# Performance work log

Hardware: AMD Instinct MI355X
Metric: run time of the kernel (lower is better)

Reference implementation:

```python
import jax, jax.numpy as jnp
import numpy as np

N, F_IN, HID, EMB, K = 4096, 1433, 256, 16, 10
ALPHA = 0.2   # LeakyReLU negative slope
V = 1.0       # Student-t degrees of freedom
NEG_INF = -9e15


def _xavier(key, shape):
    std = (2.0 / (shape[0] + shape[1])) ** 0.5
    return std * jax.random.normal(key, shape, dtype=jnp.float32)


def setup_inputs() -> dict:
    key = jax.random.key(0)
    ks = jax.random.split(key, 10)
    x = jax.random.normal(ks[0], (N, F_IN), dtype=jnp.float32)
    adj = (jax.random.uniform(ks[1], (N, N)) < 0.01).astype(jnp.float32)
    adj = jnp.maximum(adj, jnp.eye(N, dtype=jnp.float32))
    M = jax.random.uniform(ks[2], (N, N), dtype=jnp.float32)  # proximity matrix
    return {
        "x": x,
        "adj": adj,
        "M": M,
        "W1": _xavier(ks[3], (F_IN, HID)),
        "a_self1": _xavier(ks[4], (HID, 1)),
        "a_neigh1": _xavier(ks[5], (HID, 1)),
        "W2": _xavier(ks[6], (HID, EMB)),
        "a_self2": _xavier(ks[7], (EMB, 1)),
        "a_neigh2": _xavier(ks[8], (EMB, 1)),
        "cluster_layer": _xavier(ks[9], (K, EMB)),
    }


def _gat_layer(h_in, adj, M, W, a_self, a_neigh):
    h = h_in @ W                                   # [N, D]
    # dense attention logits: self score broadcast over rows + neighbor score over cols
    logits = (h @ a_self) + (h @ a_neigh).T        # [N, N]
    logits = jax.nn.leaky_relu(logits * M, negative_slope=ALPHA)
    logits = jnp.where(adj > 0, logits, NEG_INF)
    attention = jax.nn.softmax(logits, axis=1)     # row-stochastic
    return jax.nn.elu(attention @ h)               # concat=True -> ELU


def reference(x, adj, M, W1, a_self1, a_neigh1, W2, a_self2, a_neigh2, cluster_layer):
    h = _gat_layer(x, adj, M, W1, a_self1, a_neigh1)
    h = _gat_layer(h, adj, M, W2, a_self2, a_neigh2)
    # F.normalize(h, p=2, dim=1) with eps clamp
    z = h / jnp.maximum(jnp.linalg.norm(h, axis=1, keepdims=True), 1e-12)
    A_pred = jax.nn.sigmoid(z @ z.T)               # [N, N] dot-product decoder
    # Student-t soft assignment (get_Q)
    dist2 = jnp.sum((z[:, None, :] - cluster_layer[None, :, :]) ** 2, axis=2)  # [N, K]
    q = 1.0 / (1.0 + dist2 / V)
    q = q ** ((V + 1.0) / 2.0)
    q = q / jnp.sum(q, axis=1, keepdims=True)
    return A_pred, z, q
```

## Files before the change

### kernel.cpp

```cpp
#include <hip/hip_runtime.h>
#include <hip/hip_bf16.h>

#define NN 4096
#define FIN 1433
#define HID 256
#define EMB 16
#define KCL 10
#define CAP 256
#define ALPHA_LR 0.2f
#define KP 1472
#define NT (KP / 64)

typedef __attribute__((ext_vector_type(8))) short bf16x8;
typedef __attribute__((ext_vector_type(8))) short s16x8;
typedef __attribute__((ext_vector_type(4))) float f32x4;

__device__ __align__(16) short g_xb[(size_t)NN * KP];
__device__ __align__(16) short g_w1t[(size_t)HID * KP];
__device__ __align__(16) float g_h1[(size_t)NN * HID];
__device__ __align__(16) float g_s1[NN];
__device__ __align__(16) float g_n1[NN];
__device__ __align__(16) int   g_cnt[NN];
__device__ __align__(16) int   g_cols[(size_t)NN * CAP];
__device__ __align__(16) float g_mv[(size_t)NN * CAP];
__device__ __align__(16) float g_h2[(size_t)NN * EMB];
__device__ __align__(16) float g_s2[NN];
__device__ __align__(16) float g_n2[NN];
__device__ __align__(16) float g_z[(size_t)NN * EMB];

__device__ __forceinline__ short f2bf(float f) {
    union { float f; unsigned u; } v; v.f = f;
    unsigned r = v.u + 0x7fffu + ((v.u >> 16) & 1u);
    return (short)(r >> 16);
}
__device__ __forceinline__ float eluf(float v) { return v > 0.f ? v : __expf(v) - 1.f; }

__launch_bounds__(256)
__global__ void k_cast(const float* __restrict__ x, const float* __restrict__ W1) {
    int b = blockIdx.x, tid = threadIdx.x;
    if (b < NN) {
        const float* src = x + (size_t)b * FIN;
        short* dst = g_xb + (size_t)b * KP;
        for (int j = tid; j < KP; j += 256)
            dst[j] = (j < FIN) ? f2bf(src[j]) : (short)0;
    } else {
        int n = b - NN;
        short* dst = g_w1t + (size_t)n * KP;
        for (int k = tid; k < KP; k += 256)
            dst[k] = (k < FIN) ? f2bf(W1[(size_t)k * HID + n]) : (short)0;
    }
}

__launch_bounds__(256)
__global__ void k_gemm1b() {
    __shared__ short As[2][32][72];
    __shared__ short Bs[2][64][72];
    int bid = blockIdx.x;
    int rt = bid >> 2, nt = bid & 3;
    int row0 = rt * 32, n0 = nt * 64;
    int tid = threadIdx.x, lane = tid & 63, w = tid >> 6;
    int wm = w >> 1, wn = w & 1;
    int arow = tid >> 3, acol = (tid & 7) * 8;
    int brow = tid >> 2, bcol = (tid & 3) * 16;
    const short* xptr = g_xb  + (size_t)(row0 + arow) * KP + acol;
    const short* wptr = g_w1t + (size_t)(n0 + brow) * KP + bcol;
    f32x4 acc0 = {0.f,0.f,0.f,0.f}, acc1 = {0.f,0.f,0.f,0.f};

    s16x8 a_r  = *(const s16x8*)xptr;
    s16x8 b_r0 = *(const s16x8*)wptr;
    s16x8 b_r1 = *(const s16x8*)(wptr + 8);
    *(s16x8*)&As[0][arow][acol]     = a_r;
    *(s16x8*)&Bs[0][brow][bcol]     = b_r0;
    *(s16x8*)&Bs[0][brow][bcol + 8] = b_r1;
    __syncthreads();

    int fr = lane & 15, fk = (lane >> 4) * 8;
    for (int t = 0; t < NT; ++t) {
        int cur = t & 1;
        if (t + 1 < NT) {
            a_r  = *(const s16x8*)(xptr + (t + 1) * 64);
            b_r0 = *(const s16x8*)(wptr + (t + 1) * 64);
            b_r1 = *(const s16x8*)(wptr + (t + 1) * 64 + 8);
        }
        #pragma unroll
        for (int kk = 0; kk < 2; ++kk) {
            bf16x8 af  = *(const bf16x8*)&As[cur][wm * 16 + fr][fk + kk * 32];
            bf16x8 bf0 = *(const bf16x8*)&Bs[cur][wn * 32 + fr][fk + kk * 32];
            bf16x8 bf1 = *(const bf16x8*)&Bs[cur][wn * 32 + 16 + fr][fk + kk * 32];
            acc0 = __builtin_amdgcn_mfma_f32_16x16x32_bf16(af, bf0, acc0, 0, 0, 0);
            acc1 = __builtin_amdgcn_mfma_f32_16x16x32_bf16(af, bf1, acc1, 0, 0, 0);
        }
        if (t + 1 < NT) {
            *(s16x8*)&As[cur ^ 1][arow][acol]     = a_r;
            *(s16x8*)&Bs[cur ^ 1][brow][bcol]     = b_r0;
            *(s16x8*)&Bs[cur ^ 1][brow][bcol + 8] = b_r1;
            __syncthreads();
        }
    }
    int rowb = (lane >> 4) * 4;
    #pragma unroll
    for (int t = 0; t < 4; ++t) {
        int grow = row0 + wm * 16 + rowb + t;
        g_h1[(size_t)grow * HID + n0 + wn * 32 + fr]      = acc0[t];
        g_h1[(size_t)grow * HID + n0 + wn * 32 + 16 + fr] = acc1[t];
    }
}

__launch_bounds__(256)
__global__ void k_sn1(const float* __restrict__ a_s, const float* __restrict__ a_n) {
    int row = blockIdx.x * 4 + (threadIdx.x >> 6);
    int lane = threadIdx.x & 63;
    const float* r = g_h1 + (size_t)row * HID;
    float ss = 0.f, sn = 0.f;
    #pragma unroll
    for (int q = 0; q < 4; ++q) {
        float hv = r[lane + 64 * q];
        ss += hv * a_s[lane + 64 * q];
        sn += hv * a_n[lane + 64 * q];
    }
    #pragma unroll
    for (int o = 32; o; o >>= 1) { ss += __shfl_xor(ss, o); sn += __shfl_xor(sn, o); }
    if (lane == 0) { g_s1[row] = ss; g_n1[row] = sn; }
}

__launch_bounds__(256)
__global__ void k_attn1s(const float* __restrict__ adj, const float* __restrict__ M,
                         const float* __restrict__ W2,
                         const float* __restrict__ as2, const float* __restrict__ an2) {
    __shared__ int lc[4][CAP];
    __shared__ int cnts[4];
    int w = threadIdx.x >> 6, lane = threadIdx.x & 63;
    int row = blockIdx.x * 4 + w;
    if (lane == 0) cnts[w] = 0;
    __syncthreads();

    const float* Arow = adj + (size_t)row * NN;
    #pragma unroll
    for (int it = 0; it < 16; it += 8) {
        f32x4 A[8];
        #pragma unroll
        for (int u = 0; u < 8; ++u)
            A[u] = *(const f32x4*)&Arow[(it + u) * 256 + lane * 4];
        #pragma unroll
        for (int u = 0; u < 8; ++u) {
            int j0 = (it + u) * 256 + lane * 4;
            #pragma unroll
            for (int q = 0; q < 4; ++q) {
                if (A[u][q] > 0.f) {
                    int pos = atomicAdd(&cnts[w], 1);
                    if (pos < CAP) lc[w][pos] = j0 + q;
                }
            }
        }
    }
    __syncthreads();
    int nnzC = cnts[w]; if (nnzC > CAP) nnzC = CAP;
    if (lane == 0) g_cnt[row] = nnzC;

    const float* Mrow = M + (size_t)row * NN;
    float s_i = g_s1[row];
    int c0 = 0, c1 = 0;
    float lg0 = -INFINITY, lg1 = -INFINITY;
    #pragma unroll
    for (int t = 0; t < 4; ++t) {
        int k = lane + 64 * t;
        if (k < nnzC) {
            int c = lc[w][k];
            float mv = Mrow[c];
            g_cols[(size_t)row * CAP + k] = c;
            g_mv[(size_t)row * CAP + k]   = mv;
            if (t < 2) {
                float tt = (s_i + g_n1[c]) * mv;
                float lg = tt > 0.f ? tt : ALPHA_LR * tt;
                if (t == 0) { c0 = c; lg0 = lg; } else { c1 = c; lg1 = lg; }
            }
        }
    }
    int nnz = nnzC > 128 ? 128 : nnzC;

    float mx = fmaxf(lg0, lg1);
    #pragma unroll
    for (int o = 32; o; o >>= 1) mx = fmaxf(mx, __shfl_xor(mx, o));
    float p0 = (lane < nnz)      ? __expf(lg0 - mx) : 0.f;
    float p1 = (lane + 64 < nnz) ? __expf(lg1 - mx) : 0.f;
    float sm = p0 + p1;
    #pragma unroll
    for (int o = 32; o; o >>= 1) sm += __shfl_xor(sm, o);
    float inv = 1.f / sm;

    f32x4 acc = {0.f, 0.f, 0.f, 0.f};
    int kmax = nnz < 64 ? nnz : 64;
    #pragma unroll 4
    for (int k = 0; k < kmax; ++k) {
        float p = __shfl(p0, k);
        int   c = __shfl(c0, k);
        acc += p * *(const f32x4*)&g_h1[(size_t)c * HID + lane * 4];
    }
    if (nnz > 64) {
        int k2 = nnz - 64;
        #pragma unroll 4
        for (int k = 0; k < k2; ++k) {
            float p = __shfl(p1, k);
            int   c = __shfl(c1, k);
            acc += p * *(const f32x4*)&g_h1[(size_t)c * HID + lane * 4];
        }
    }
    f32x4 o1;
    #pragma unroll
    for (int j = 0; j < 4; ++j) o1[j] = eluf(acc[j] * inv);

    float part[16];
    #pragma unroll
    for (int e = 0; e < 16; ++e) part[e] = 0.f;
    #pragma unroll
    for (int j = 0; j < 4; ++j) {
        const f32x4* wr = (const f32x4*)&W2[(size_t)(lane * 4 + j) * EMB];
        f32x4 w0 = wr[0], w1 = wr[1], w2 = wr[2], w3 = wr[3];
        float ov = o1[j];
        #pragma unroll
        for (int e = 0; e < 4; ++e) {
            part[e]      += ov * w0[e];
            part[4 + e]  += ov * w1[e];
            part[8 + e]  += ov * w2[e];
            part[12 + e] += ov * w3[e];
        }
    }
    #pragma unroll
    for (int o = 32; o; o >>= 1)
        #pragma unroll
        for (int e = 0; e < 16; ++e) part[e] += __shfl_xor(part[e], o);
    if (lane == 0) {
        float ps = 0.f, pn = 0.f;
        float* h2p = g_h2 + (size_t)row * EMB;
        #pragma unroll
        for (int e = 0; e < 16; ++e) {
            h2p[e] = part[e];
            ps += part[e] * as2[e];
            pn += part[e] * an2[e];
        }
        g_s2[row] = ps; g_n2[row] = pn;
    }
}

__launch_bounds__(256)
__global__ void k_attn2s(const float* __restrict__ cl,
                         float* __restrict__ zo, float* __restrict__ qo) {
    int row = blockIdx.x * 4 + (threadIdx.x >> 6);
    int lane = threadIdx.x & 63;
    int kq = lane >> 4, c = lane & 15;
    int nnz = g_cnt[row];
    float s_i = g_s2[row];
    const int* cp = g_cols + (size_t)row * CAP;
    const float* mp = g_mv + (size_t)row * CAP;
    float mx = -INFINITY;
    for (int k = kq; k < nnz; k += 4) {
        float t = (s_i + g_n2[cp[k]]) * mp[k];
        mx = fmaxf(mx, t > 0.f ? t : ALPHA_LR * t);
    }
    mx = fmaxf(mx, __shfl_xor(mx, 16));
    mx = fmaxf(mx, __shfl_xor(mx, 32));
    float l = 0.f, acc = 0.f;
    for (int k = kq; k < nnz; k += 4) {
        int colk = cp[k];
        float t = (s_i + g_n2[colk]) * mp[k];
        float p = __expf((t > 0.f ? t : ALPHA_LR * t) - mx);
        l += p;
        acc += p * g_h2[(size_t)colk * EMB + c];
    }
    l += __shfl_xor(l, 16);  l += __shfl_xor(l, 32);
    acc += __shfl_xor(acc, 16); acc += __shfl_xor(acc, 32);
    float h = eluf(acc / l);
    float ss = h * h;
    ss += __shfl_xor(ss, 1); ss += __shfl_xor(ss, 2);
    ss += __shfl_xor(ss, 4); ss += __shfl_xor(ss, 8);
    float z = h * (1.f / fmaxf(sqrtf(ss), 1e-12f));
    if (kq == 0) { g_z[(size_t)row * EMB + c] = z; zo[(size_t)row * EMB + c] = z; }
    float qv[KCL]; float qs = 0.f;
    #pragma unroll
    for (int k2 = 0; k2 < KCL; ++k2) {
        float d = z - cl[k2 * EMB + c];
        float d2 = d * d;
        d2 += __shfl_xor(d2, 1); d2 += __shfl_xor(d2, 2);
        d2 += __shfl_xor(d2, 4); d2 += __shfl_xor(d2, 8);
        float t = 1.f / (1.f + d2);
        qv[k2] = t; qs += t;
    }
    if (kq == 0 && c < KCL) {
        float myq = 0.f;
        #pragma unroll
        for (int k2 = 0; k2 < KCL; ++k2) if (c == k2) myq = qv[k2];
        qo[(size_t)row * KCL + c] = myq / qs;
    }
}

__launch_bounds__(256)
__global__ void k_apred(float* __restrict__ out) {
    __shared__ float za[128][17];
    __shared__ float zb[128][17];
    int bx = blockIdx.x & 31, by = blockIdx.x >> 5;
    int tid = threadIdx.x;
    {
        int idx = tid * 8;
        int row = idx >> 4;
        int e = idx & 15;
        const f32x4* sa = (const f32x4*)(g_z + (size_t)(by * 128 + row) * EMB + e);
        const f32x4* sb = (const f32x4*)(g_z + (size_t)(bx * 128 + row) * EMB + e);
        f32x4 a0 = sa[0], a1 = sa[1], b0 = sb[0], b1 = sb[1];
        #pragma unroll
        for (int t = 0; t < 4; ++t) {
            za[row][e + t] = a0[t]; za[row][e + 4 + t] = a1[t];
            zb[row][e + t] = b0[t]; zb[row][e + 4 + t] = b1[t];
        }
    }
    __syncthreads();
    int tr = tid >> 4, tc = tid & 15;
    float acc[8][8];
    #pragma unroll
    for (int r = 0; r < 8; ++r)
        #pragma unroll
        for (int c = 0; c < 8; ++c) acc[r][c] = 0.f;
    for (int e = 0; e < 16; ++e) {
        float ra[8], rb[8];
        #pragma unroll
        for (int r = 0; r < 8; ++r) ra[r] = za[tr * 8 + r][e];
        #pragma unroll
        for (int c = 0; c < 8; ++c) rb[c] = zb[tc * 8 + c][e];
        #pragma unroll
        for (int r = 0; r < 8; ++r)
            #pragma unroll
            for (int c = 0; c < 8; ++c) acc[r][c] += ra[r] * rb[c];
    }
    #pragma unroll
    for (int r = 0; r < 8; ++r) {
        f32x4 lo, hi;
        #pragma unroll
        for (int c = 0; c < 4; ++c) {
            lo[c] = 1.f / (1.f + __expf(-acc[r][c]));
            hi[c] = 1.f / (1.f + __expf(-acc[r][c + 4]));
        }
        float* dst = &out[(size_t)(by * 128 + tr * 8 + r) * NN + bx * 128 + tc * 8];
        *(f32x4*)dst = lo;
        *(f32x4*)(dst + 4) = hi;
    }
}

extern "C" void kernel_launch(void* const* d_in, const int* in_sizes, int n_in,
                              void* d_out, int out_size, void* d_ws, size_t ws_size,
                              hipStream_t stream) {
    (void)in_sizes; (void)n_in; (void)d_ws; (void)ws_size; (void)out_size;
    const float* x   = (const float*)d_in[0];
    const float* adj = (const float*)d_in[1];
    const float* M   = (const float*)d_in[2];
    const float* W1  = (const float*)d_in[3];
    const float* as1 = (const float*)d_in[4];
    const float* an1 = (const float*)d_in[5];
    const float* W2  = (const float*)d_in[6];
    const float* as2 = (const float*)d_in[7];
    const float* an2 = (const float*)d_in[8];
    const float* cl  = (const float*)d_in[9];

    float* outA = (float*)d_out;
    float* outZ = outA + (size_t)NN * NN;
    float* outQ = outZ + (size_t)NN * EMB;

    hipLaunchKernelGGL(k_cast,   dim3(NN + HID), dim3(256), 0, stream, x, W1);
    hipLaunchKernelGGL(k_gemm1b, dim3(512),      dim3(256), 0, stream);
    hipLaunchKernelGGL(k_sn1,    dim3(1024),     dim3(256), 0, stream, as1, an1);
    hipLaunchKernelGGL(k_attn1s, dim3(1024),     dim3(256), 0, stream, adj, M, W2, as2, an2);
    hipLaunchKernelGGL(k_attn2s, dim3(1024),     dim3(256), 0, stream, cl, outZ, outQ);
    hipLaunchKernelGGL(k_apred,  dim3(1024),     dim3(256), 0, stream, outA);
}
```

Baseline: 261.7 us.

## Assign one workgroup per row in first-layer attention kernel

The first attention kernel moves from one wavefront per row (four rows per block) to a full 256-thread block per row, with 4096 blocks launched instead of 1024. The adjacency scan, the logit and softmax reductions, and the sparse gather of neighbour h1 rows are now split across four wavefronts, and partial results are combined through shared memory. The aim is more memory-level parallelism on the long per-row adjacency read and the neighbour gather. The cost is extra __syncthreads barriers, shared-memory round trips, and a W2 projection done by one wave while the other three sit idle.

```diff
diff --git a/kernel.cpp b/kernel.cpp
--- a/kernel.cpp
+++ b/kernel.cpp
@@ -127,118 +127,110 @@
 __global__ void k_attn1s(const float* __restrict__ adj, const float* __restrict__ M,
                          const float* __restrict__ W2,
                          const float* __restrict__ as2, const float* __restrict__ an2) {
-    __shared__ int lc[4][CAP];
-    __shared__ int cnts[4];
-    int w = threadIdx.x >> 6, lane = threadIdx.x & 63;
-    int row = blockIdx.x * 4 + w;
-    if (lane == 0) cnts[w] = 0;
+    __shared__ int   lc[CAP];
+    __shared__ float P[128];
+    __shared__ float o1p[4][256];
+    __shared__ float redm[4], reds[4];
+    __shared__ int   cnt;
+    int tid = threadIdx.x, lane = tid & 63, w = tid >> 6;
+    int row = blockIdx.x;
+    if (tid == 0) cnt = 0;
     __syncthreads();
 
     const float* Arow = adj + (size_t)row * NN;
-    #pragma unroll
-    for (int it = 0; it < 16; it += 8) {
-        f32x4 A[8];
-        #pragma unroll
-        for (int u = 0; u < 8; ++u)
-            A[u] = *(const f32x4*)&Arow[(it + u) * 256 + lane * 4];
-        #pragma unroll
-        for (int u = 0; u < 8; ++u) {
-            int j0 = (it + u) * 256 + lane * 4;
-            #pragma unroll
-            for (int q = 0; q < 4; ++q) {
-                if (A[u][q] > 0.f) {
-                    int pos = atomicAdd(&cnts[w], 1);
-                    if (pos < CAP) lc[w][pos] = j0 + q;
-                }
+    f32x4 A0 = *(const f32x4*)&Arow[tid * 4];
+    f32x4 A1 = *(const f32x4*)&Arow[1024 + tid * 4];
+    f32x4 A2 = *(const f32x4*)&Arow[2048 + tid * 4];
+    f32x4 A3 = *(const f32x4*)&Arow[3072 + tid * 4];
+    f32x4 blk[4] = {A0, A1, A2, A3};
+    #pragma unroll
+    for (int u = 0; u < 4; ++u)
+        #pragma unroll
+        for (int q = 0; q < 4; ++q)
+            if (blk[u][q] > 0.f) {
+                int pos = atomicAdd(&cnt, 1);
+                if (pos < CAP) lc[pos] = u * 1024 + tid * 4 + q;
             }
-        }
-    }
-    __syncthreads();
-    int nnzC = cnts[w]; if (nnzC > CAP) nnzC = CAP;
-    if (lane == 0) g_cnt[row] = nnzC;
+    __syncthreads();
+    int nnzC = cnt > CAP ? CAP : cnt;
+    if (tid == 0) g_cnt[row] = nnzC;
+    int nnz = nnzC > 128 ? 128 : nnzC;
 
     const float* Mrow = M + (size_t)row * NN;
     float s_i = g_s1[row];
-    int c0 = 0, c1 = 0;
-    float lg0 = -INFINITY, lg1 = -INFINITY;
-    #pragma unroll
-    for (int t = 0; t < 4; ++t) {
-        int k = lane + 64 * t;
-        if (k < nnzC) {
-            int c = lc[w][k];
-            float mv = Mrow[c];
-            g_cols[(size_t)row * CAP + k] = c;
-            g_mv[(size_t)row * CAP + k]   = mv;
-            if (t < 2) {
-                float tt = (s_i + g_n1[c]) * mv;
-                float lg = tt > 0.f ? tt : ALPHA_LR * tt;
-                if (t == 0) { c0 = c; lg0 = lg; } else { c1 = c; lg1 = lg; }
+    float lg = -INFINITY;
+    if (tid < nnzC) {
+        int c = lc[tid];
+        float mv = Mrow[c];
+        g_cols[(size_t)row * CAP + tid] = c;
+        g_mv[(size_t)row * CAP + tid]   = mv;
+        if (tid < 128) {
+            float t = (s_i + g_n1[c]) * mv;
+            lg = t > 0.f ? t : ALPHA_LR * t;
+        }
+    }
+    float mx = lg;
+    #pragma unroll
+    for (int o = 32; o; o >>= 1) mx = fmaxf(mx, __shfl_xor(mx, o));
+    if (lane == 0) redm[w] = mx;
+    __syncthreads();
+    mx = fmaxf(fmaxf(redm[0], redm[1]), fmaxf(redm[2], redm[3]));
+    float p = (tid < nnz) ? __expf(lg - mx) : 0.f;
+    if (tid < 128) P[tid] = p;
+    float sm = p;
+    #pragma unroll
+    for (int o = 32; o; o >>= 1) sm += __shfl_xor(sm, o);
+    if (lane == 0) reds[w] = sm;
+    __syncthreads();
+    float inv = 1.f / (reds[0] + reds[1] + reds[2] + reds[3]);
+
+    f32x4 acc = {0.f, 0.f, 0.f, 0.f};
+    #pragma unroll 2
+    for (int k = w; k < nnz; k += 4) {
+        float pk = P[k];
+        int   c  = lc[k];
+        acc += pk * *(const f32x4*)&g_h1[(size_t)c * HID + lane * 4];
+    }
+    *(f32x4*)&o1p[w][lane * 4] = acc;
+    __syncthreads();
+    float o1v = (o1p[0][tid] + o1p[1][tid]) + (o1p[2][tid] + o1p[3][tid]);
+    o1v = eluf(o1v * inv);
+    __syncthreads();
+    o1p[0][tid] = o1v;
+    __syncthreads();
+
+    if (w == 0) {
+        float part[16];
+        #pragma unroll
+        for (int e = 0; e < 16; ++e) part[e] = 0.f;
+        #pragma unroll
+        for (int j = 0; j < 4; ++j) {
+            float ov = o1p[0][lane * 4 + j];
+            const f32x4* wr = (const f32x4*)&W2[(size_t)(lane * 4 + j) * EMB];
+            f32x4 w0 = wr[0], w1 = wr[1], w2 = wr[2], w3 = wr[3];
+            #pragma unroll
+            for (int e = 0; e < 4; ++e) {
+                part[e]      += ov * w0[e];
+                part[4 + e]  += ov * w1[e];
+                part[8 + e]  += ov * w2[e];
+                part[12 + e] += ov * w3[e];
             }
         }
-    }
-    int nnz = nnzC > 128 ? 128 : nnzC;
-
-    float mx = fmaxf(lg0, lg1);
-    #pragma unroll
-    for (int o = 32; o; o >>= 1) mx = fmaxf(mx, __shfl_xor(mx, o));
-    float p0 = (lane < nnz)      ? __expf(lg0 - mx) : 0.f;
-    float p1 = (lane + 64 < nnz) ? __expf(lg1 - mx) : 0.f;
-    float sm = p0 + p1;
-    #pragma unroll
-    for (int o = 32; o; o >>= 1) sm += __shfl_xor(sm, o);
-    float inv = 1.f / sm;
-
-    f32x4 acc = {0.f, 0.f, 0.f, 0.f};
-    int kmax = nnz < 64 ? nnz : 64;
-    #pragma unroll 4
-    for (int k = 0; k < kmax; ++k) {
-        float p = __shfl(p0, k);
-        int   c = __shfl(c0, k);
-        acc += p * *(const f32x4*)&g_h1[(size_t)c * HID + lane * 4];
-    }
-    if (nnz > 64) {
-        int k2 = nnz - 64;
-        #pragma unroll 4
-        for (int k = 0; k < k2; ++k) {
-            float p = __shfl(p1, k);
-            int   c = __shfl(c1, k);
-            acc += p * *(const f32x4*)&g_h1[(size_t)c * HID + lane * 4];
-        }
-    }
-    f32x4 o1;
-    #pragma unroll
-    for (int j = 0; j < 4; ++j) o1[j] = eluf(acc[j] * inv);
-
-    float part[16];
-    #pragma unroll
-    for (int e = 0; e < 16; ++e) part[e] = 0.f;
-    #pragma unroll
-    for (int j = 0; j < 4; ++j) {
-        const f32x4* wr = (const f32x4*)&W2[(size_t)(lane * 4 + j) * EMB];
-        f32x4 w0 = wr[0], w1 = wr[1], w2 = wr[2], w3 = wr[3];
-        float ov = o1[j];
-        #pragma unroll
-        for (int e = 0; e < 4; ++e) {
-            part[e]      += ov * w0[e];
-            part[4 + e]  += ov * w1[e];
-            part[8 + e]  += ov * w2[e];
-            part[12 + e] += ov * w3[e];
-        }
-    }
-    #pragma unroll
-    for (int o = 32; o; o >>= 1)
-        #pragma unroll
-        for (int e = 0; e < 16; ++e) part[e] += __shfl_xor(part[e], o);
-    if (lane == 0) {
-        float ps = 0.f, pn = 0.f;
-        float* h2p = g_h2 + (size_t)row * EMB;
-        #pragma unroll
-        for (int e = 0; e < 16; ++e) {
-            h2p[e] = part[e];
-            ps += part[e] * as2[e];
-            pn += part[e] * an2[e];
-        }
-        g_s2[row] = ps; g_n2[row] = pn;
+        #pragma unroll
+        for (int o = 32; o; o >>= 1)
+            #pragma unroll
+            for (int e = 0; e < 16; ++e) part[e] += __shfl_xor(part[e], o);
+        if (lane == 0) {
+            float ps = 0.f, pn = 0.f;
+            float* h2p = g_h2 + (size_t)row * EMB;
+            #pragma unroll
+            for (int e = 0; e < 16; ++e) {
+                h2p[e] = part[e];
+                ps += part[e] * as2[e];
+                pn += part[e] * an2[e];
+            }
+            g_s2[row] = ps; g_n2[row] = pn;
+        }
     }
 }
 
@@ -366,7 +358,7 @@
     hipLaunchKernelGGL(k_cast,   dim3(NN + HID), dim3(256), 0, stream, x, W1);
     hipLaunchKernelGGL(k_gemm1b, dim3(512),      dim3(256), 0, stream);
     hipLaunchKernelGGL(k_sn1,    dim3(1024),     dim3(256), 0, stream, as1, an1);
-    hipLaunchKernelGGL(k_attn1s, dim3(1024),     dim3(256), 0, stream, adj, M, W2, as2, an2);
+    hipLaunchKernelGGL(k_attn1s, dim3(4096),     dim3(256), 0, stream, adj, M, W2, as2, an2);
     hipLaunchKernelGGL(k_attn2s, dim3(1024),     dim3(256), 0, stream, cl, outZ, outQ);
     hipLaunchKernelGGL(k_apred,  dim3(1024),     dim3(256), 0, stream, outA);
 }
```

Result: faster. 256.5 us (-2.0%).
